# Performance work log

Hardware: AMD Instinct MI355X
Metric: run time of the kernel (lower is better)

Reference implementation:

```python
import jax, jax.numpy as jnp
import numpy as np

TOP_K = 2
NUM_EXPERTS = 8

def setup_inputs() -> dict:
    key = jax.random.key(0)
    k_x, k_r, k_g, k_u, k_d = jax.random.split(key, 5)
    B, L, D, H, E = 1, 2048, 1024, 2048, NUM_EXPERTS
    scale = 0.02  # keep router logits / activations in a sane range
    return {
        "x": jax.random.normal(k_x, (B, L, D), dtype=jnp.float32),
        "router_w": jax.random.normal(k_r, (D, E), dtype=jnp.float32) * scale,
        "gate_w": jax.random.normal(k_g, (E, D, H), dtype=jnp.float32) * scale,
        "up_w": jax.random.normal(k_u, (E, D, H), dtype=jnp.float32) * scale,
        "down_w": jax.random.normal(k_d, (E, H, D), dtype=jnp.float32) * scale,
    }

def reference(x, router_w, gate_w, up_w, down_w):
    # x: (B, L, D)
    B, L, D = x.shape
    T = B * L
    E = router_w.shape[1]
    xf = x.reshape(T, D)

    # --- router: top-k softmax over selected logits (Mixtral-style) ---
    logits = xf @ router_w                      # (T, E)
    top_vals, top_idx = jax.lax.top_k(logits, TOP_K)  # (T, K)
    top_w = jax.nn.softmax(top_vals, axis=-1)   # (T, K)

    # combine weights scattered to dense (T, E); zeros for unrouted experts
    combine = jnp.zeros((T, E), dtype=x.dtype).at[
        jnp.arange(T)[:, None], top_idx
    ].add(top_w)

    # --- experts: SwiGLU, computed per expert, zero-weight tokens masked by combine ---
    gate = jnp.einsum('td,edh->eth', xf, gate_w)   # (E, T, H)
    up = jnp.einsum('td,edh->eth', xf, up_w)       # (E, T, H)
    hidden = jax.nn.silu(gate) * up                # (E, T, H)
    expert_out = jnp.einsum('eth,ehd->etd', hidden, down_w)  # (E, T, D)

    # --- weighted combine (equivalent to scatter_add over sorted assignments) ---
    y = jnp.einsum('etd,te->td', expert_out, combine)  # (T, D)
    return y.reshape(B, L, D)
```

## Files before the change

### kernel.cpp

```cpp
#include <hip/hip_runtime.h>
#include <hip/hip_bf16.h>
#include <stdint.h>

#define T_TOK 2048
#define DIM   1024
#define HDIM  2048
#define NE    8
#define ROWS_PAD 4224
#define TSLOTS 40

typedef __attribute__((ext_vector_type(8))) short bf16x8;
typedef __attribute__((ext_vector_type(4))) float f32x4;

__device__ __forceinline__ unsigned short f2bf(float f) {
    union { float f; unsigned int u; } v; v.f = f;
    unsigned int r = v.u + 0x7FFF + ((v.u >> 16) & 1);
    return (unsigned short)(r >> 16);
}

__device__ __forceinline__ float bf2f(unsigned short b) {
    union { unsigned int u; float f; } v; v.u = ((unsigned int)b) << 16;
    return v.f;
}

__device__ __forceinline__ void gload16(const void* g, void* l) {
    __builtin_amdgcn_global_load_lds(
        (const __attribute__((address_space(1))) void*)g,
        (__attribute__((address_space(3))) void*)l, 16, 0, 0);
}

__global__ void transpose_cvt(const float* __restrict__ in, unsigned short* __restrict__ out,
                              int R, int C) {
    __shared__ float tile[32][33];
    int b = blockIdx.z;
    int bx = blockIdx.x, by = blockIdx.y;
    int tx = threadIdx.x & 31, ty = threadIdx.x >> 5;
    const float* ip = in + (size_t)b * R * C;
    unsigned short* op = out + (size_t)b * R * C;
#pragma unroll
    for (int i = 0; i < 4; ++i) {
        int r = by * 32 + ty + i * 8;
        tile[ty + i * 8][tx] = ip[(size_t)r * C + bx * 32 + tx];
    }
    __syncthreads();
#pragma unroll
    for (int i = 0; i < 2; ++i) {
        int oc = i * 16 + (threadIdx.x >> 4);
        int orw2 = (threadIdx.x & 15) * 2;
        ushort2 v;
        v.x = f2bf(tile[orw2][oc]);
        v.y = f2bf(tile[orw2 + 1][oc]);
        *(ushort2*)&op[(size_t)(bx * 32 + oc) * R + by * 32 + orw2] = v;
    }
}

__global__ void router_kernel(const float* __restrict__ x, const float* __restrict__ rw,
                              int* __restrict__ counts, int* __restrict__ top_idx,
                              float* __restrict__ top_w) {
    int wid = (blockIdx.x * blockDim.x + threadIdx.x) >> 6;
    int lane = threadIdx.x & 63;
    if (wid >= T_TOK) return;
    float acc[NE];
#pragma unroll
    for (int e = 0; e < NE; ++e) acc[e] = 0.f;
    const float* xr = x + (size_t)wid * DIM;
    for (int i = lane; i < DIM; i += 64) {
        float xv = xr[i];
        const float* wr = rw + (size_t)i * NE;
#pragma unroll
        for (int e = 0; e < NE; ++e) acc[e] += xv * wr[e];
    }
#pragma unroll
    for (int off = 32; off; off >>= 1) {
#pragma unroll
        for (int e = 0; e < NE; ++e) acc[e] += __shfl_xor(acc[e], off, 64);
    }
    if (lane == 0) {
        float v0 = -1e30f, v1 = -1e30f; int i0 = 0, i1 = 0;
#pragma unroll
        for (int e = 0; e < NE; ++e) {
            float v = acc[e];
            if (v > v0) { v1 = v0; i1 = i0; v0 = v; i0 = e; }
            else if (v > v1) { v1 = v; i1 = e; }
        }
        float e1 = __expf(v1 - v0);
        float s = 1.f + e1;
        top_idx[wid * 2]     = i0;
        top_idx[wid * 2 + 1] = i1;
        top_w[wid * 2]     = 1.f / s;
        top_w[wid * 2 + 1] = e1 / s;
        atomicAdd(&counts[i0], 1);
        atomicAdd(&counts[i1], 1);
    }
}

__global__ void scan_kernel(const int* __restrict__ counts, int* __restrict__ offsets,
                            int* __restrict__ cursors,
                            int* __restrict__ tl_e, int* __restrict__ tl_m) {
    if (threadIdx.x == 0) {
        int run = 0;
        for (int e = 0; e < NE; ++e) { offsets[e] = run; cursors[e] = run; run += counts[e]; }
        int n = 0;
        for (int e = 0; e < NE; ++e) {
            int mt = (counts[e] + 127) >> 7;
            for (int m = 0; m < mt && n < 64; ++m) { tl_e[n] = e; tl_m[n] = m; ++n; }
        }
        for (; n < 64; ++n) tl_e[n] = -1;
    }
}

__global__ void gather_kernel(const float* __restrict__ x, const int* __restrict__ top_idx,
                              const float* __restrict__ top_w, int* __restrict__ cursors,
                              int* __restrict__ row_tok, float* __restrict__ row_w,
                              unsigned short* __restrict__ Abuf) {
    int t = blockIdx.x;
    __shared__ int pos[2];
    if (threadIdx.x < 2) {
        int k = threadIdx.x;
        int e = top_idx[t * 2 + k];
        int p = atomicAdd(&cursors[e], 1);
        pos[k] = p;
        row_tok[p] = t;
        row_w[p] = top_w[t * 2 + k];
    }
    __syncthreads();
    const float4* xr = (const float4*)(x + (size_t)t * DIM);
    float4 v = xr[threadIdx.x];
    ushort4 b;
    b.x = f2bf(v.x); b.y = f2bf(v.y); b.z = f2bf(v.z); b.w = f2bf(v.w);
    ushort4* A4 = (ushort4*)Abuf;
    A4[(size_t)pos[0] * (DIM / 4) + threadIdx.x] = b;
    A4[(size_t)pos[1] * (DIM / 4) + threadIdx.x] = b;
}

__global__ __launch_bounds__(256, 4)
void gemm1_kernel(const unsigned short* __restrict__ Abuf,
                  const unsigned short* __restrict__ WgT,
                  const unsigned short* __restrict__ WuT,
                  unsigned short* __restrict__ Hbuf,
                  const int* __restrict__ offsets, const int* __restrict__ counts,
                  const int* __restrict__ tl_e, const int* __restrict__ tl_m) {
    const int slot = blockIdx.y;
    const int e = tl_e[slot];
    if (e < 0) return;
    const int mtile = tl_m[slot];
    const int cnt = counts[e];
    const int n0 = blockIdx.x * 64;
    const int row0 = offsets[e] + mtile * 128;

    __shared__ __align__(16) unsigned char lds_raw[32768];
    unsigned short* AsB = (unsigned short*)lds_raw;
    unsigned short* BgB = (unsigned short*)(lds_raw + 16384);
    unsigned short* BuB = (unsigned short*)(lds_raw + 24576);
    unsigned short* ex  = (unsigned short*)lds_raw;

    const int tid = threadIdx.x;
    const int lane = tid & 63;
    const int wave = tid >> 6;
    const int wm = wave >> 1;
    const int wu = wave & 1;

    f32x4 acc[4][4];
#pragma unroll
    for (int i = 0; i < 4; ++i)
#pragma unroll
        for (int j = 0; j < 4; ++j) acc[i][j] = (f32x4){0.f, 0.f, 0.f, 0.f};

    const int srow = tid >> 2;
    const int sc0 = tid & 3;
    const unsigned short* Aab = Abuf + (size_t)row0 * DIM;
    const unsigned short* Bgb = WgT + (size_t)e * HDIM * DIM + (size_t)n0 * DIM;
    const unsigned short* Bub = WuT + (size_t)e * HDIM * DIM + (size_t)n0 * DIM;

    auto stage = [&](int buf, int kt) {
#pragma unroll
        for (int i = 0; i < 2; ++i) {
            int row = i * 64 + srow;
            int csrc = sc0 ^ ((row >> 1) & 3);
            gload16(Aab + (size_t)row * DIM + kt + csrc * 8,
                    AsB + buf * 4096 + (i * 256 + tid) * 8);
        }
        int csrcb = sc0 ^ ((srow >> 1) & 3);
        gload16(Bgb + (size_t)srow * DIM + kt + csrcb * 8, BgB + buf * 2048 + tid * 8);
        gload16(Bub + (size_t)srow * DIM + kt + csrcb * 8, BuB + buf * 2048 + tid * 8);
    };

    const int rsel = lane & 15;
    const int csrcf = lane >> 4;

    stage(0, 0);
    int cur = 0;
    for (int kt = 0; kt < DIM; kt += 32) {
        __syncthreads();
        if (kt + 32 < DIM) stage(cur ^ 1, kt + 32);
        const unsigned short* Ac = AsB + cur * 4096;
        const unsigned short* Bc = (wu ? BuB : BgB) + cur * 2048;
        bf16x8 af[4], bb[4];
#pragma unroll
        for (int i = 0; i < 4; ++i) {
            int ra = wm * 64 + i * 16 + rsel;
            af[i] = *(const bf16x8*)&Ac[ra * 32 + (csrcf ^ ((ra >> 1) & 3)) * 8];
            int rb = i * 16 + rsel;
            bb[i] = *(const bf16x8*)&Bc[rb * 32 + (csrcf ^ ((rb >> 1) & 3)) * 8];
        }
#pragma unroll
        for (int i = 0; i < 4; ++i)
#pragma unroll
            for (int j = 0; j < 4; ++j)
                acc[i][j] = __builtin_amdgcn_mfma_f32_16x16x32_bf16(af[i], bb[j], acc[i][j], 0, 0, 0);
        cur ^= 1;
    }

    const int c = lane & 15, rbase = (lane >> 4) * 4;
    const int obase = offsets[e];
    __syncthreads();
    if (wu) {
#pragma unroll
        for (int i = 0; i < 4; ++i)
#pragma unroll
            for (int r = 0; r < 4; ++r) {
                int row64 = i * 16 + rbase + r;
#pragma unroll
                for (int j = 0; j < 4; ++j)
                    ex[wm * 4096 + row64 * 64 + j * 16 + c] = f2bf(acc[i][j][r]);
            }
    }
    __syncthreads();
    if (!wu) {
#pragma unroll
        for (int i = 0; i < 4; ++i) {
#pragma unroll
            for (int r = 0; r < 4; ++r) {
                int row64 = i * 16 + rbase + r;
                int lrow = mtile * 128 + wm * 64 + row64;
                if (lrow < cnt) {
                    size_t orow = (size_t)(obase + lrow);
#pragma unroll
                    for (int j = 0; j < 4; ++j) {
                        float g = acc[i][j][r];
                        float u = bf2f(ex[wm * 4096 + row64 * 64 + j * 16 + c]);
                        float h = g * u / (1.f + __expf(-g));
                        Hbuf[orow * HDIM + n0 + j * 16 + c] = f2bf(h);
                    }
                }
            }
        }
    }
}

__global__ __launch_bounds__(256, 3)
void gemm2_kernel(const unsigned short* __restrict__ Hbuf,
                  const unsigned short* __restrict__ WdT,
                  float* __restrict__ y,
                  const int* __restrict__ offsets, const int* __restrict__ counts,
                  const int* __restrict__ row_tok, const float* __restrict__ row_w,
                  const int* __restrict__ tl_e, const int* __restrict__ tl_m) {
    const int slot = blockIdx.y;
    const int e = tl_e[slot];
    if (e < 0) return;
    const int mtile = tl_m[slot];
    const int kc = blockIdx.z;
    const int cnt = counts[e];
    const int n0 = blockIdx.x * 128;
    const int row0 = offsets[e] + mtile * 128;

    __shared__ unsigned short As[3][128 * 32];
    __shared__ unsigned short Bs[3][128 * 32];

    const int tid = threadIdx.x;
    const int lane = tid & 63;
    const int wave = tid >> 6;
    const int wm = wave >> 1, wn = wave & 1;

    f32x4 acc[4][4];
#pragma unroll
    for (int i = 0; i < 4; ++i)
#pragma unroll
        for (int j = 0; j < 4; ++j) acc[i][j] = (f32x4){0.f, 0.f, 0.f, 0.f};

    const int srow0 = tid >> 2;
    const int sc0 = tid & 3;
    const unsigned short* Aab = Hbuf + (size_t)row0 * HDIM;
    const unsigned short* Bbb = WdT + (size_t)e * DIM * HDIM + (size_t)n0 * HDIM;

    auto stage = [&](int buf, int kt) {
#pragma unroll
        for (int i = 0; i < 2; ++i) {
            int row = i * 64 + srow0;
            int csrc = sc0 ^ ((row >> 1) & 3);
            size_t go = (size_t)row * HDIM + kt + csrc * 8;
            int lo = (i * 256 + tid) * 8;
            gload16(Aab + go, &As[buf][lo]);
            gload16(Bbb + go, &Bs[buf][lo]);
        }
    };

    const int rsel = lane & 15;
    const int csrcf = lane >> 4;

    const int kbeg = kc * (HDIM / 2);
    const int NS = (HDIM / 2) / 32;

    stage(0, kbeg);
    stage(1, kbeg + 32);
    int cur = 0;
    for (int s = 0; s < NS; ++s) {
        if (s + 1 < NS) { asm volatile("s_waitcnt vmcnt(4)" ::: "memory"); }
        else            { asm volatile("s_waitcnt vmcnt(0)" ::: "memory"); }
        __builtin_amdgcn_s_barrier();
        if (s + 2 < NS) {
            int pb = cur + 2; if (pb >= 3) pb -= 3;
            stage(pb, kbeg + (s + 2) * 32);
        }
        const unsigned short* Ac = As[cur];
        const unsigned short* Bc = Bs[cur];
        bf16x8 af[4], bf[4];
#pragma unroll
        for (int i = 0; i < 4; ++i) {
            int ra = wm * 64 + i * 16 + rsel;
            af[i] = *(const bf16x8*)&Ac[ra * 32 + (csrcf ^ ((ra >> 1) & 3)) * 8];
            int rb = wn * 64 + i * 16 + rsel;
            bf[i] = *(const bf16x8*)&Bc[rb * 32 + (csrcf ^ ((rb >> 1) & 3)) * 8];
        }
#pragma unroll
        for (int i = 0; i < 4; ++i)
#pragma unroll
            for (int j = 0; j < 4; ++j)
                acc[i][j] = __builtin_amdgcn_mfma_f32_16x16x32_bf16(af[i], bf[j], acc[i][j], 0, 0, 0);
        ++cur; if (cur == 3) cur = 0;
    }

    const int c = lane & 15, rbase = (lane >> 4) * 4;
    const int obase = offsets[e];
#pragma unroll
    for (int i = 0; i < 4; ++i) {
#pragma unroll
        for (int r = 0; r < 4; ++r) {
            int lrow = mtile * 128 + wm * 64 + i * 16 + rbase + r;
            if (lrow < cnt) {
                int grow = obase + lrow;
                int tok = row_tok[grow];
                float w = row_w[grow];
#pragma unroll
                for (int j = 0; j < 4; ++j) {
                    atomicAdd(&y[(size_t)tok * DIM + n0 + wn * 64 + j * 16 + c], w * acc[i][j][r]);
                }
            }
        }
    }
}

extern "C" void kernel_launch(void* const* d_in, const int* in_sizes, int n_in,
                              void* d_out, int out_size, void* d_ws, size_t ws_size,
                              hipStream_t stream) {
    const float* x  = (const float*)d_in[0];
    const float* rw = (const float*)d_in[1];
    const float* gw = (const float*)d_in[2];
    const float* uw = (const float*)d_in[3];
    const float* dw = (const float*)d_in[4];
    float* y = (float*)d_out;

    char* ws = (char*)d_ws;
    int*   counts  = (int*)(ws + 0);
    int*   cursors = (int*)(ws + 32);
    int*   offsets = (int*)(ws + 64);
    int*   top_idx = (int*)(ws + 128);
    float* top_w   = (float*)(ws + 128 + 16384);
    int*   row_tok = (int*)(ws + 128 + 32768);
    float* row_w   = (float*)(ws + 128 + 32768 + 16896);
    int*   tl_e    = (int*)(ws + 128 + 32768 + 2 * 16896);
    int*   tl_m    = (int*)(ws + 128 + 32768 + 2 * 16896 + 256);
    size_t off = 128 + 32768 + 2 * 16896 + 512;
    off = (off + 255) & ~(size_t)255;
    unsigned short* Abuf = (unsigned short*)(ws + off); off += (size_t)ROWS_PAD * DIM * 2;
    unsigned short* Hbuf = (unsigned short*)(ws + off); off += (size_t)ROWS_PAD * HDIM * 2;
    unsigned short* WgT  = (unsigned short*)(ws + off); off += (size_t)NE * DIM * HDIM * 2;
    unsigned short* WuT  = (unsigned short*)(ws + off); off += (size_t)NE * DIM * HDIM * 2;
    unsigned short* WdT  = (unsigned short*)(ws + off); off += (size_t)NE * DIM * HDIM * 2;
    if (ws_size < off) return;

    hipMemsetAsync(counts, 0, 32, stream);
    hipMemsetAsync(d_out, 0, (size_t)out_size * 4, stream);

    transpose_cvt<<<dim3(HDIM / 32, DIM / 32, NE), 256, 0, stream>>>(gw, WgT, DIM, HDIM);
    transpose_cvt<<<dim3(HDIM / 32, DIM / 32, NE), 256, 0, stream>>>(uw, WuT, DIM, HDIM);
    transpose_cvt<<<dim3(DIM / 32, HDIM / 32, NE), 256, 0, stream>>>(dw, WdT, HDIM, DIM);

    router_kernel<<<T_TOK / 4, 256, 0, stream>>>(x, rw, counts, top_idx, top_w);
    scan_kernel<<<1, 64, 0, stream>>>(counts, offsets, cursors, tl_e, tl_m);
    gather_kernel<<<T_TOK, 256, 0, stream>>>(x, top_idx, top_w, cursors, row_tok, row_w, Abuf);

    gemm1_kernel<<<dim3(HDIM / 64, TSLOTS), 256, 0, stream>>>(Abuf, WgT, WuT, Hbuf,
                                                              offsets, counts, tl_e, tl_m);
    gemm2_kernel<<<dim3(DIM / 128, TSLOTS, 2), 256, 0, stream>>>(Hbuf, WdT, y, offsets, counts,
                                                                 row_tok, row_w, tl_e, tl_m);
}
```

Measured before the change: 269.6 us.

## Fuse weight transposes with router and deepen GEMM K-tiles to 64

Merges the three weight transpose/convert launches and the router into one prep kernel, removing launch gaps and letting the router blocks run alongside the transpose blocks. Both expert GEMMs switch to a BK of 64 with an 8-way XOR swizzle and two MFMA k-substeps per barrier, which halves the number of barriers per tile. gemm2 also drops from a 3-stage vmcnt-controlled pipeline to a plain double buffer. The larger LDS footprint lowers the occupancy target to 2 blocks per CU, trading latency hiding for fewer syncs.

```diff
diff --git a/kernel.cpp b/kernel.cpp
--- a/kernel.cpp
+++ b/kernel.cpp
@@ -29,68 +29,77 @@
         (__attribute__((address_space(3))) void*)l, 16, 0, 0);
 }
 
-__global__ void transpose_cvt(const float* __restrict__ in, unsigned short* __restrict__ out,
-                              int R, int C) {
+#define NTT (3 * 16384)
+__global__ void prep_kernel(const float* __restrict__ gw, const float* __restrict__ uw,
+                            const float* __restrict__ dw,
+                            unsigned short* __restrict__ WgT, unsigned short* __restrict__ WuT,
+                            unsigned short* __restrict__ WdT,
+                            const float* __restrict__ x, const float* __restrict__ rw,
+                            int* __restrict__ counts, int* __restrict__ top_idx,
+                            float* __restrict__ top_w) {
     __shared__ float tile[32][33];
-    int b = blockIdx.z;
-    int bx = blockIdx.x, by = blockIdx.y;
-    int tx = threadIdx.x & 31, ty = threadIdx.x >> 5;
-    const float* ip = in + (size_t)b * R * C;
-    unsigned short* op = out + (size_t)b * R * C;
-#pragma unroll
-    for (int i = 0; i < 4; ++i) {
-        int r = by * 32 + ty + i * 8;
-        tile[ty + i * 8][tx] = ip[(size_t)r * C + bx * 32 + tx];
-    }
-    __syncthreads();
-#pragma unroll
-    for (int i = 0; i < 2; ++i) {
-        int oc = i * 16 + (threadIdx.x >> 4);
-        int orw2 = (threadIdx.x & 15) * 2;
-        ushort2 v;
-        v.x = f2bf(tile[orw2][oc]);
-        v.y = f2bf(tile[orw2 + 1][oc]);
-        *(ushort2*)&op[(size_t)(bx * 32 + oc) * R + by * 32 + orw2] = v;
-    }
-}
-
-__global__ void router_kernel(const float* __restrict__ x, const float* __restrict__ rw,
-                              int* __restrict__ counts, int* __restrict__ top_idx,
-                              float* __restrict__ top_w) {
-    int wid = (blockIdx.x * blockDim.x + threadIdx.x) >> 6;
-    int lane = threadIdx.x & 63;
-    if (wid >= T_TOK) return;
-    float acc[NE];
-#pragma unroll
-    for (int e = 0; e < NE; ++e) acc[e] = 0.f;
-    const float* xr = x + (size_t)wid * DIM;
-    for (int i = lane; i < DIM; i += 64) {
-        float xv = xr[i];
-        const float* wr = rw + (size_t)i * NE;
-#pragma unroll
-        for (int e = 0; e < NE; ++e) acc[e] += xv * wr[e];
-    }
-#pragma unroll
-    for (int off = 32; off; off >>= 1) {
-#pragma unroll
-        for (int e = 0; e < NE; ++e) acc[e] += __shfl_xor(acc[e], off, 64);
-    }
-    if (lane == 0) {
-        float v0 = -1e30f, v1 = -1e30f; int i0 = 0, i1 = 0;
-#pragma unroll
-        for (int e = 0; e < NE; ++e) {
-            float v = acc[e];
-            if (v > v0) { v1 = v0; i1 = i0; v0 = v; i0 = e; }
-            else if (v > v1) { v1 = v; i1 = e; }
-        }
-        float e1 = __expf(v1 - v0);
-        float s = 1.f + e1;
-        top_idx[wid * 2]     = i0;
-        top_idx[wid * 2 + 1] = i1;
-        top_w[wid * 2]     = 1.f / s;
-        top_w[wid * 2 + 1] = e1 / s;
-        atomicAdd(&counts[i0], 1);
-        atomicAdd(&counts[i1], 1);
+    const int b = blockIdx.x;
+    if (b < NTT) {
+        const int m = b >> 14;
+        const int t = b & 16383;
+        const int e = t >> 11;
+        const int rem = t & 2047;
+        const float* in; unsigned short* out; int R, C, by, bx;
+        if (m == 0)      { in = gw; out = WgT; R = DIM;  C = HDIM; by = rem >> 6; bx = rem & 63; }
+        else if (m == 1) { in = uw; out = WuT; R = DIM;  C = HDIM; by = rem >> 6; bx = rem & 63; }
+        else             { in = dw; out = WdT; R = HDIM; C = DIM;  by = rem >> 5; bx = rem & 31; }
+        const float* ip = in + (size_t)e * R * C;
+        unsigned short* op = out + (size_t)e * R * C;
+        const int tx = threadIdx.x & 31, ty = threadIdx.x >> 5;
+#pragma unroll
+        for (int i = 0; i < 4; ++i)
+            tile[ty + i * 8][tx] = ip[(size_t)(by * 32 + ty + i * 8) * C + bx * 32 + tx];
+        __syncthreads();
+#pragma unroll
+        for (int i = 0; i < 2; ++i) {
+            int oc = i * 16 + (threadIdx.x >> 4);
+            int orw2 = (threadIdx.x & 15) * 2;
+            ushort2 v;
+            v.x = f2bf(tile[orw2][oc]);
+            v.y = f2bf(tile[orw2 + 1][oc]);
+            *(ushort2*)&op[(size_t)(bx * 32 + oc) * R + by * 32 + orw2] = v;
+        }
+    } else {
+        const int wid = (b - NTT) * 4 + (threadIdx.x >> 6);
+        const int lane = threadIdx.x & 63;
+        if (wid >= T_TOK) return;
+        float acc[NE];
+#pragma unroll
+        for (int e = 0; e < NE; ++e) acc[e] = 0.f;
+        const float* xr = x + (size_t)wid * DIM;
+        for (int i = lane; i < DIM; i += 64) {
+            float xv = xr[i];
+            const float* wr = rw + (size_t)i * NE;
+#pragma unroll
+            for (int e = 0; e < NE; ++e) acc[e] += xv * wr[e];
+        }
+#pragma unroll
+        for (int off = 32; off; off >>= 1) {
+#pragma unroll
+            for (int e = 0; e < NE; ++e) acc[e] += __shfl_xor(acc[e], off, 64);
+        }
+        if (lane == 0) {
+            float v0 = -1e30f, v1 = -1e30f; int i0 = 0, i1 = 0;
+#pragma unroll
+            for (int e = 0; e < NE; ++e) {
+                float v = acc[e];
+                if (v > v0) { v1 = v0; i1 = i0; v0 = v; i0 = e; }
+                else if (v > v1) { v1 = v; i1 = e; }
+            }
+            float e1 = __expf(v1 - v0);
+            float s = 1.f + e1;
+            top_idx[wid * 2]     = i0;
+            top_idx[wid * 2 + 1] = i1;
+            top_w[wid * 2]     = 1.f / s;
+            top_w[wid * 2 + 1] = e1 / s;
+            atomicAdd(&counts[i0], 1);
+            atomicAdd(&counts[i1], 1);
+        }
     }
 }
 
@@ -133,7 +142,7 @@
     A4[(size_t)pos[1] * (DIM / 4) + threadIdx.x] = b;
 }
 
-__global__ __launch_bounds__(256, 4)
+__global__ __launch_bounds__(256, 2)
 void gemm1_kernel(const unsigned short* __restrict__ Abuf,
                   const unsigned short* __restrict__ WgT,
                   const unsigned short* __restrict__ WuT,
@@ -148,10 +157,10 @@
     const int n0 = blockIdx.x * 64;
     const int row0 = offsets[e] + mtile * 128;
 
-    __shared__ __align__(16) unsigned char lds_raw[32768];
+    __shared__ __align__(16) unsigned char lds_raw[65536];
     unsigned short* AsB = (unsigned short*)lds_raw;
-    unsigned short* BgB = (unsigned short*)(lds_raw + 16384);
-    unsigned short* BuB = (unsigned short*)(lds_raw + 24576);
+    unsigned short* BgB = (unsigned short*)(lds_raw + 32768);
+    unsigned short* BuB = (unsigned short*)(lds_raw + 49152);
     unsigned short* ex  = (unsigned short*)lds_raw;
 
     const int tid = threadIdx.x;
@@ -166,23 +175,28 @@
 #pragma unroll
         for (int j = 0; j < 4; ++j) acc[i][j] = (f32x4){0.f, 0.f, 0.f, 0.f};
 
-    const int srow = tid >> 2;
-    const int sc0 = tid & 3;
+    const int srow = tid >> 3;
+    const int sc0 = tid & 7;
     const unsigned short* Aab = Abuf + (size_t)row0 * DIM;
     const unsigned short* Bgb = WgT + (size_t)e * HDIM * DIM + (size_t)n0 * DIM;
     const unsigned short* Bub = WuT + (size_t)e * HDIM * DIM + (size_t)n0 * DIM;
 
     auto stage = [&](int buf, int kt) {
 #pragma unroll
+        for (int i = 0; i < 4; ++i) {
+            int row = i * 32 + srow;
+            int csrc = sc0 ^ (row & 7);
+            gload16(Aab + (size_t)row * DIM + kt + csrc * 8,
+                    AsB + buf * 8192 + (i * 256 + tid) * 8);
+        }
+#pragma unroll
         for (int i = 0; i < 2; ++i) {
-            int row = i * 64 + srow;
-            int csrc = sc0 ^ ((row >> 1) & 3);
-            gload16(Aab + (size_t)row * DIM + kt + csrc * 8,
-                    AsB + buf * 4096 + (i * 256 + tid) * 8);
-        }
-        int csrcb = sc0 ^ ((srow >> 1) & 3);
-        gload16(Bgb + (size_t)srow * DIM + kt + csrcb * 8, BgB + buf * 2048 + tid * 8);
-        gload16(Bub + (size_t)srow * DIM + kt + csrcb * 8, BuB + buf * 2048 + tid * 8);
+            int row = i * 32 + srow;
+            int csrc = sc0 ^ (row & 7);
+            size_t go = (size_t)row * DIM + kt + csrc * 8;
+            gload16(Bgb + go, BgB + buf * 4096 + (i * 256 + tid) * 8);
+            gload16(Bub + go, BuB + buf * 4096 + (i * 256 + tid) * 8);
+        }
     };
 
     const int rsel = lane & 15;
@@ -190,24 +204,27 @@
 
     stage(0, 0);
     int cur = 0;
-    for (int kt = 0; kt < DIM; kt += 32) {
+    for (int kt = 0; kt < DIM; kt += 64) {
         __syncthreads();
-        if (kt + 32 < DIM) stage(cur ^ 1, kt + 32);
-        const unsigned short* Ac = AsB + cur * 4096;
-        const unsigned short* Bc = (wu ? BuB : BgB) + cur * 2048;
-        bf16x8 af[4], bb[4];
-#pragma unroll
-        for (int i = 0; i < 4; ++i) {
-            int ra = wm * 64 + i * 16 + rsel;
-            af[i] = *(const bf16x8*)&Ac[ra * 32 + (csrcf ^ ((ra >> 1) & 3)) * 8];
-            int rb = i * 16 + rsel;
-            bb[i] = *(const bf16x8*)&Bc[rb * 32 + (csrcf ^ ((rb >> 1) & 3)) * 8];
-        }
-#pragma unroll
-        for (int i = 0; i < 4; ++i)
-#pragma unroll
-            for (int j = 0; j < 4; ++j)
-                acc[i][j] = __builtin_amdgcn_mfma_f32_16x16x32_bf16(af[i], bb[j], acc[i][j], 0, 0, 0);
+        if (kt + 64 < DIM) stage(cur ^ 1, kt + 64);
+        const unsigned short* Ac = AsB + cur * 8192;
+        const unsigned short* Bc = (wu ? BuB : BgB) + cur * 4096;
+#pragma unroll
+        for (int kk = 0; kk < 2; ++kk) {
+            bf16x8 af[4], bb[4];
+#pragma unroll
+            for (int i = 0; i < 4; ++i) {
+                int ra = wm * 64 + i * 16 + rsel;
+                af[i] = *(const bf16x8*)&Ac[ra * 64 + ((kk * 4 + csrcf) ^ (ra & 7)) * 8];
+                int rb = i * 16 + rsel;
+                bb[i] = *(const bf16x8*)&Bc[rb * 64 + ((kk * 4 + csrcf) ^ (rb & 7)) * 8];
+            }
+#pragma unroll
+            for (int i = 0; i < 4; ++i)
+#pragma unroll
+                for (int j = 0; j < 4; ++j)
+                    acc[i][j] = __builtin_amdgcn_mfma_f32_16x16x32_bf16(af[i], bb[j], acc[i][j], 0, 0, 0);
+        }
         cur ^= 1;
     }
 
@@ -248,7 +265,7 @@
     }
 }
 
-__global__ __launch_bounds__(256, 3)
+__global__ __launch_bounds__(256, 2)
 void gemm2_kernel(const unsigned short* __restrict__ Hbuf,
                   const unsigned short* __restrict__ WdT,
                   float* __restrict__ y,
@@ -264,8 +281,8 @@
     const int n0 = blockIdx.x * 128;
     const int row0 = offsets[e] + mtile * 128;
 
-    __shared__ unsigned short As[3][128 * 32];
-    __shared__ unsigned short Bs[3][128 * 32];
+    __shared__ unsigned short As[2][128 * 64];
+    __shared__ unsigned short Bs[2][128 * 64];
 
     const int tid = threadIdx.x;
     const int lane = tid & 63;
@@ -278,16 +295,16 @@
 #pragma unroll
         for (int j = 0; j < 4; ++j) acc[i][j] = (f32x4){0.f, 0.f, 0.f, 0.f};
 
-    const int srow0 = tid >> 2;
-    const int sc0 = tid & 3;
+    const int srow0 = tid >> 3;
+    const int sc0 = tid & 7;
     const unsigned short* Aab = Hbuf + (size_t)row0 * HDIM;
     const unsigned short* Bbb = WdT + (size_t)e * DIM * HDIM + (size_t)n0 * HDIM;
 
     auto stage = [&](int buf, int kt) {
 #pragma unroll
-        for (int i = 0; i < 2; ++i) {
-            int row = i * 64 + srow0;
-            int csrc = sc0 ^ ((row >> 1) & 3);
+        for (int i = 0; i < 4; ++i) {
+            int row = i * 32 + srow0;
+            int csrc = sc0 ^ (row & 7);
             size_t go = (size_t)row * HDIM + kt + csrc * 8;
             int lo = (i * 256 + tid) * 8;
             gload16(Aab + go, &As[buf][lo]);
@@ -299,35 +316,32 @@
     const int csrcf = lane >> 4;
 
     const int kbeg = kc * (HDIM / 2);
-    const int NS = (HDIM / 2) / 32;
+    const int kend = kbeg + (HDIM / 2);
 
     stage(0, kbeg);
-    stage(1, kbeg + 32);
     int cur = 0;
-    for (int s = 0; s < NS; ++s) {
-        if (s + 1 < NS) { asm volatile("s_waitcnt vmcnt(4)" ::: "memory"); }
-        else            { asm volatile("s_waitcnt vmcnt(0)" ::: "memory"); }
-        __builtin_amdgcn_s_barrier();
-        if (s + 2 < NS) {
-            int pb = cur + 2; if (pb >= 3) pb -= 3;
-            stage(pb, kbeg + (s + 2) * 32);
-        }
+    for (int kt = kbeg; kt < kend; kt += 64) {
+        __syncthreads();
+        if (kt + 64 < kend) stage(cur ^ 1, kt + 64);
         const unsigned short* Ac = As[cur];
         const unsigned short* Bc = Bs[cur];
-        bf16x8 af[4], bf[4];
-#pragma unroll
-        for (int i = 0; i < 4; ++i) {
-            int ra = wm * 64 + i * 16 + rsel;
-            af[i] = *(const bf16x8*)&Ac[ra * 32 + (csrcf ^ ((ra >> 1) & 3)) * 8];
-            int rb = wn * 64 + i * 16 + rsel;
-            bf[i] = *(const bf16x8*)&Bc[rb * 32 + (csrcf ^ ((rb >> 1) & 3)) * 8];
-        }
-#pragma unroll
-        for (int i = 0; i < 4; ++i)
-#pragma unroll
-            for (int j = 0; j < 4; ++j)
-                acc[i][j] = __builtin_amdgcn_mfma_f32_16x16x32_bf16(af[i], bf[j], acc[i][j], 0, 0, 0);
-        ++cur; if (cur == 3) cur = 0;
+#pragma unroll
+        for (int kk = 0; kk < 2; ++kk) {
+            bf16x8 af[4], bf[4];
+#pragma unroll
+            for (int i = 0; i < 4; ++i) {
+                int ra = wm * 64 + i * 16 + rsel;
+                af[i] = *(const bf16x8*)&Ac[ra * 64 + ((kk * 4 + csrcf) ^ (ra & 7)) * 8];
+                int rb = wn * 64 + i * 16 + rsel;
+                bf[i] = *(const bf16x8*)&Bc[rb * 64 + ((kk * 4 + csrcf) ^ (rb & 7)) * 8];
+            }
+#pragma unroll
+            for (int i = 0; i < 4; ++i)
+#pragma unroll
+                for (int j = 0; j < 4; ++j)
+                    acc[i][j] = __builtin_amdgcn_mfma_f32_16x16x32_bf16(af[i], bf[j], acc[i][j], 0, 0, 0);
+        }
+        cur ^= 1;
     }
 
     const int c = lane & 15, rbase = (lane >> 4) * 4;
@@ -382,11 +396,8 @@
     hipMemsetAsync(counts, 0, 32, stream);
     hipMemsetAsync(d_out, 0, (size_t)out_size * 4, stream);
 
-    transpose_cvt<<<dim3(HDIM / 32, DIM / 32, NE), 256, 0, stream>>>(gw, WgT, DIM, HDIM);
-    transpose_cvt<<<dim3(HDIM / 32, DIM / 32, NE), 256, 0, stream>>>(uw, WuT, DIM, HDIM);
-    transpose_cvt<<<dim3(DIM / 32, HDIM / 32, NE), 256, 0, stream>>>(dw, WdT, HDIM, DIM);
-
-    router_kernel<<<T_TOK / 4, 256, 0, stream>>>(x, rw, counts, top_idx, top_w);
+    prep_kernel<<<NTT + T_TOK / 4, 256, 0, stream>>>(gw, uw, dw, WgT, WuT, WdT,
+                                                     x, rw, counts, top_idx, top_w);
     scan_kernel<<<1, 64, 0, stream>>>(counts, offsets, cursors, tl_e, tl_m);
     gather_kernel<<<T_TOK, 256, 0, stream>>>(x, top_idx, top_w, cursors, row_tok, row_w, Abuf);
 
```

Measured after the change: 262.7 us. -2.6%, faster.
